# Kernel tuning notes

Hardware: AMD Instinct MI355X
Metric: run time of the kernel (lower is better)

The kernel has to match this reference:

```python
import jax, jax.numpy as jnp
import numpy as np

ACT_BITS = 8
W_BITS = 8
BN_EPS = 1e-5


def _round_ste(x):
    # straight-through round (HAWQ-style ste_round)
    return x + jax.lax.stop_gradient(jnp.round(x) - x)


def _quant_sym(x, bits):
    # symmetric per-tensor fake quantization; scale treated as constant (EMA min/max in original)
    n = float(2 ** (bits - 1) - 1)
    s = jax.lax.stop_gradient(jnp.maximum(jnp.max(jnp.abs(x)) / n, 1e-8))
    xq = jnp.clip(_round_ste(x / s), -n - 1.0, n) * s
    return xq, s


def _conv(x, w, stride, pad):
    return jax.lax.conv_general_dilated(
        x, w, (stride, stride), [(pad, pad), (pad, pad)],
        dimension_numbers=("NCHW", "OIHW", "NCHW"))


def _quant_bn(x, gamma, beta, mean, var):
    # fold BN into a per-channel scale+bias; quantize the folded scale like a weight
    ws = gamma * jax.lax.rsqrt(var + BN_EPS)          # [C]
    wq, ws_scale = _quant_sym(ws, W_BITS)
    b = beta - mean * wq                               # [C]
    return x * wq[None, :, None, None] + b[None, :, None, None], ws_scale


def setup_inputs() -> dict:
    key = jax.random.key(0)
    ks = jax.random.split(key, 16)
    d = {}
    d["x"] = jax.random.normal(ks[0], (32, 128, 56, 56), jnp.float32)
    d["w1"] = jax.random.normal(ks[1], (256, 128, 3, 3), jnp.float32) * 0.05
    d["w2"] = jax.random.normal(ks[2], (256, 256, 3, 3), jnp.float32) * 0.05
    d["w_id"] = jax.random.normal(ks[3], (256, 128, 1, 1), jnp.float32) * 0.05
    for i, pfx in enumerate(["bn1", "bn2", "id"]):
        k4 = jax.random.split(ks[4 + i], 4)
        d[pfx + "_gamma"] = jax.random.uniform(k4[0], (256,), jnp.float32) + 0.5
        d[pfx + "_beta"] = jax.random.normal(k4[1], (256,), jnp.float32) * 0.1
        d[pfx + "_mean"] = jax.random.normal(k4[2], (256,), jnp.float32) * 0.1
        d[pfx + "_var"] = jax.random.uniform(k4[3], (256,), jnp.float32) + 0.5
    return d


def reference(x, w1, w2, w_id,
              bn1_gamma, bn1_beta, bn1_mean, bn1_var,
              bn2_gamma, bn2_beta, bn2_mean, bn2_var,
              id_gamma, id_beta, id_mean, id_var):
    # quant_act on block input
    xq, act_s = _quant_sym(x, ACT_BITS)

    # identity branch: 1x1 stride-2 quantized conv -> quant_act -> folded quant bn
    w_id_q, _ = _quant_sym(w_id, W_BITS)
    identity = _conv(xq, w_id_q, 2, 0)
    identity, _ = _quant_sym(identity, ACT_BITS)
    identity, _ = _quant_bn(identity, id_gamma, id_beta, id_mean, id_var)

    # main branch conv1 (3x3 stride 2) -> act quant -> bn -> relu -> act quant
    w1_q, _ = _quant_sym(w1, W_BITS)
    h = _conv(xq, w1_q, 2, 1)
    h, _ = _quant_sym(h, ACT_BITS)
    h, _ = _quant_bn(h, bn1_gamma, bn1_beta, bn1_mean, bn1_var)
    h = jax.nn.relu(h)
    h, _ = _quant_sym(h, ACT_BITS)

    # conv2 (3x3 stride 1) -> act quant -> bn
    w2_q, _ = _quant_sym(w2, W_BITS)
    h = _conv(h, w2_q, 1, 1)
    h, _ = _quant_sym(h, ACT_BITS)
    h, _ = _quant_bn(h, bn2_gamma, bn2_beta, bn2_mean, bn2_var)

    # residual add -> int32 requant -> relu
    h = h + identity
    h, out_s = _quant_sym(h, ACT_BITS)
    h = jax.nn.relu(h)
    return h, out_s
```

## Files before the change

### kernel.cpp

```cpp
#include <hip/hip_runtime.h>
#include <limits.h>

#define THREADS 256

typedef int vi4 __attribute__((ext_vector_type(4)));

__device__ __forceinline__ float clamp8f(float q) { return fminf(fmaxf(q, -128.0f), 127.0f); }
__device__ __forceinline__ float sc_from_bits(unsigned b) {
  return fmaxf(__uint_as_float(b) / 127.0f, 1e-8f);
}
__device__ __forceinline__ signed char q8(float v, float s) {
  return (signed char)(int)clamp8f(rintf(v / s));
}


__device__ __forceinline__ void amax_body(const float4* __restrict__ p, int n4, int bid,
                                          int nblocks, int* __restrict__ slot) {
  const int tid = threadIdx.x;
  const int stride = nblocks * THREADS;
  float m = 0.0f;
  int i = bid * THREADS + tid;
  for (; i + 3 * stride < n4; i += 4 * stride) {
    float4 v0 = p[i];
    float4 v1 = p[i + stride];
    float4 v2 = p[i + 2 * stride];
    float4 v3 = p[i + 3 * stride];
    float m0 = fmaxf(fmaxf(fabsf(v0.x), fabsf(v0.y)), fmaxf(fabsf(v0.z), fabsf(v0.w)));
    float m1 = fmaxf(fmaxf(fabsf(v1.x), fabsf(v1.y)), fmaxf(fabsf(v1.z), fabsf(v1.w)));
    float m2 = fmaxf(fmaxf(fabsf(v2.x), fabsf(v2.y)), fmaxf(fabsf(v2.z), fabsf(v2.w)));
    float m3 = fmaxf(fmaxf(fabsf(v3.x), fabsf(v3.y)), fmaxf(fabsf(v3.z), fabsf(v3.w)));
    m = fmaxf(m, fmaxf(fmaxf(m0, m1), fmaxf(m2, m3)));
  }
  for (; i < n4; i += stride) {
    float4 v = p[i];
    m = fmaxf(m, fmaxf(fmaxf(fabsf(v.x), fabsf(v.y)), fmaxf(fabsf(v.z), fabsf(v.w))));
  }
#pragma unroll
  for (int k = 32; k >= 1; k >>= 1) m = fmaxf(m, __shfl_xor(m, k));
  __shared__ float wred[4];
  if ((tid & 63) == 0) wred[tid >> 6] = m;
  __syncthreads();
  if (tid == 0) {
    m = fmaxf(fmaxf(wred[0], wred[1]), fmaxf(wred[2], wred[3]));
    atomicMax(slot, __float_as_int(m));
  }
}

__global__ __launch_bounds__(THREADS) void k_pre(
    int* IS, const float* g1, const float* be1, const float* m1, const float* v1, float* wq1,
    float* b1, const float* g2, const float* be2, const float* m2, const float* v2, float* wq2,
    float* b2, const float* gi, const float* bei, const float* mi, const float* vvi, float* wqi,
    float* bi, const float4* w1, const float4* w2, const float4* wid, const float4* x) {
  int b = blockIdx.x;
  int c = threadIdx.x;
  if (b < 3) {
    const float *gamma, *beta, *mean, *var;
    float *wq, *bb;
    if (b == 0) { gamma = g1; beta = be1; mean = m1; var = v1; wq = wq1; bb = b1; }
    else if (b == 1) { gamma = g2; beta = be2; mean = m2; var = v2; wq = wq2; bb = b2; }
    else { gamma = gi; beta = bei; mean = mi; var = vvi; wq = wqi; bb = bi; }
    __shared__ float red[THREADS];
    float ws = gamma[c] * (1.0f / sqrtf(var[c] + 1e-5f));
    red[c] = fabsf(ws);
    __syncthreads();
    for (int s = THREADS / 2; s > 0; s >>= 1) {
      if (c < s) red[c] = fmaxf(red[c], red[c + s]);
      __syncthreads();
    }
    float sws = fmaxf(red[0] / 127.0f, 1e-8f);
    float q = clamp8f(rintf(ws / sws)) * sws;
    wq[c] = q;
    bb[c] = beta[c] - mean[c] * q;
    return;
  }
  b -= 3;
  if (b < 64) { amax_body(w1, 73728, b, 64, IS + 1); return; }
  b -= 64;
  if (b < 128) { amax_body(w2, 147456, b, 128, IS + 2); return; }
  b -= 128;
  if (b < 16) { amax_body(wid, 8192, b, 16, IS + 3); return; }
  b -= 16;
  amax_body(x, 3211264, b, 512, IS + 0);
}

__global__ __launch_bounds__(THREADS) void k_quant(const float* __restrict__ x,
                                                   int* __restrict__ X8,
                                                   const float* __restrict__ w1f,
                                                   vi4* __restrict__ W1m,
                                                   const float* __restrict__ w2f,
                                                   vi4* __restrict__ W2m,
                                                   const float* __restrict__ widf,
                                                   vi4* __restrict__ Widm,
                                                   const unsigned* __restrict__ ISu) {
  __shared__ signed char tile[56 * 132];
  int b = blockIdx.x;
  int t = threadIdx.x;
  if (b < 1792) {
    float s = sc_from_bits(ISu[0]);
    int h = b % 56, n = b / 56;
    const float* xp = x + ((n * 128) * 56 + h) * 56;
#pragma unroll
    for (int k = 0; k < 28; ++k) {
      int i = t + k * 256;
      int w = i % 56, c = i / 56;
      tile[w * 132 + c] = q8(xp[c * 3136 + w], s);
    }
    __syncthreads();
    int* op = X8 + (n * 56 + h) * 56 * 32;
#pragma unroll
    for (int k = 0; k < 7; ++k) {
      int i = t + k * 256;
      int w = i >> 5, c4 = (i & 31) * 4;
      const signed char* tp = tile + w * 132 + c4;
      op[i] = (int)(unsigned char)tp[0] | ((int)(unsigned char)tp[1] << 8) |
              ((int)(unsigned char)tp[2] << 16) | ((int)(unsigned char)tp[3] << 24);
    }
    return;
  }
  if (b < 1864) {
    int tt = (b - 1792) * THREADS + t;
    float s = sc_from_bits(ISu[1]);
    int lane = tt & 63;
    int cotile = (tt >> 6) & 15;
    int ks = tt >> 10;
    int tap = ks >> 1, kc = ks & 1;
    int kh = tap / 3, kw = tap % 3;
    int co = cotile * 16 + (lane & 15);
    int ci0 = kc * 64 + (lane >> 4) * 16;
    const float* src = w1f + (co * 128 + ci0) * 9 + kh * 3 + kw;
    int r[4];
#pragma unroll
    for (int q = 0; q < 4; ++q) {
      unsigned b0 = (unsigned char)q8(src[(q * 4 + 0) * 9], s);
      unsigned b1 = (unsigned char)q8(src[(q * 4 + 1) * 9], s);
      unsigned b2 = (unsigned char)q8(src[(q * 4 + 2) * 9], s);
      unsigned b3 = (unsigned char)q8(src[(q * 4 + 3) * 9], s);
      r[q] = (int)(b0 | (b1 << 8) | (b2 << 16) | (b3 << 24));
    }
    vi4 v = {r[0], r[1], r[2], r[3]};
    W1m[tt] = v;
    return;
  }
  if (b < 2008) {
    int tt = (b - 1864) * THREADS + t;
    float s = sc_from_bits(ISu[2]);
    int lane = tt & 63;
    int cotile = (tt >> 6) & 15;
    int ks = tt >> 10;
    int tap = ks >> 2, kc = ks & 3;
    int kh = tap / 3, kw = tap % 3;
    int co = cotile * 16 + (lane & 15);
    int ci0 = kc * 64 + (lane >> 4) * 16;
    const float* src = w2f + (co * 256 + ci0) * 9 + kh * 3 + kw;
    int r[4];
#pragma unroll
    for (int q = 0; q < 4; ++q) {
      unsigned b0 = (unsigned char)q8(src[(q * 4 + 0) * 9], s);
      unsigned b1 = (unsigned char)q8(src[(q * 4 + 1) * 9], s);
      unsigned b2 = (unsigned char)q8(src[(q * 4 + 2) * 9], s);
      unsigned b3 = (unsigned char)q8(src[(q * 4 + 3) * 9], s);
      r[q] = (int)(b0 | (b1 << 8) | (b2 << 16) | (b3 << 24));
    }
    vi4 v = {r[0], r[1], r[2], r[3]};
    W2m[tt] = v;
    return;
  }
  {
    int tt = (b - 2008) * THREADS + t;
    float s = sc_from_bits(ISu[3]);
    int lane = tt & 63;
    int cotile = (tt >> 6) & 15;
    int ks = tt >> 10;
    int co = cotile * 16 + (lane & 15);
    int ci0 = ks * 64 + (lane >> 4) * 16;
    const float* src = widf + co * 128 + ci0;
    int r[4];
#pragma unroll
    for (int q = 0; q < 4; ++q) {
      unsigned b0 = (unsigned char)q8(src[q * 4 + 0], s);
      unsigned b1 = (unsigned char)q8(src[q * 4 + 1], s);
      unsigned b2 = (unsigned char)q8(src[q * 4 + 2], s);
      unsigned b3 = (unsigned char)q8(src[q * 4 + 3], s);
      r[q] = (int)(b0 | (b1 << 8) | (b2 << 16) | (b3 << 24));
    }
    vi4 v = {r[0], r[1], r[2], r[3]};
    Widm[tt] = v;
  }
}

#define MFMA_I8(a, b, c) __builtin_amdgcn_mfma_i32_16x16x64_i8(a, b, c, 0, 0, 0)

__global__ __launch_bounds__(THREADS, 3) void k_conv1(const int* __restrict__ X8,
                                                      const vi4* __restrict__ W1m,
                                                      const vi4* __restrict__ Widm,
                                                      int* __restrict__ H1, int* __restrict__ IDI,
                                                      int* __restrict__ maxS,
                                                      int* __restrict__ minS,
                                                      int* __restrict__ maxabs_id) {
  __shared__ __align__(16) int lds[5 * 58 * 36];
  __shared__ int sMax[2][128], sMin[2][128], redA[4];
  const int tid = threadIdx.x;
  const int bx = blockIdx.x;
  const int n = bx / 28, rr = bx % 28;
  const int hp = rr >> 1, nh = rr & 1;
  const int ho0 = hp * 2;
  vi4 zero = {0, 0, 0, 0};

  for (int r = 0; r < 5; ++r) {
    int h = 2 * ho0 - 1 + r;
    int* dst = lds + r * 58 * 36;
    if (h >= 0 && h < 56) {
      const vi4* src = (const vi4*)(X8 + (n * 56 + h) * 56 * 32);
      for (int i4 = tid; i4 < 448; i4 += THREADS) {
        int col = i4 >> 3, c = (i4 & 7) * 4;
        *(vi4*)(dst + (col + 1) * 36 + c) = src[i4];
      }
      if (tid < 32) dst[tid] = 0;
      else if (tid >= 128 && tid < 160) dst[57 * 36 + (tid - 128)] = 0;
    } else {
      for (int i4 = tid; i4 < 522; i4 += THREADS) ((vi4*)dst)[i4] = zero;
    }
  }
  __syncthreads();

  const int lane = tid & 63, wv = tid >> 6;
  const int mw = wv & 1, nw = wv >> 1;
  const int lm = lane & 15, quad = lane >> 4;
  const int woc0 = lm, woc1 = (16 + lm) > 27 ? 27 : (16 + lm);
  const int choff = quad * 4;
  const int ho = ho0 + mw;
  const int obase = ((n * 28 + ho) * 28) * 256;
  const int ctbase = nh * 8 + nw * 4;

  vi4 acc[2][4];
  vi4 bA[4], bB[4];
  vi4 a0A, a1A, a0B, a1B;

#pragma unroll
  for (int mt = 0; mt < 2; ++mt)
#pragma unroll
    for (int ct = 0; ct < 4; ++ct) acc[mt][ct] = zero;
  const vi4* wibase = Widm + ctbase * 64 + lane;
  {
    const int ro = (2 * mw + 1) * 58;
#pragma unroll
    for (int kc = 0; kc < 2; ++kc) {
      vi4 a0 = *(const vi4*)(lds + (ro + 2 * woc0 + 1) * 36 + kc * 16 + choff);
      vi4 a1 = *(const vi4*)(lds + (ro + 2 * woc1 + 1) * 36 + kc * 16 + choff);
#pragma unroll
      for (int ct = 0; ct < 4; ++ct) {
        vi4 b = wibase[kc * 1024 + ct * 64];
        acc[0][ct] = MFMA_I8(a0, b, acc[0][ct]);
        acc[1][ct] = MFMA_I8(a1, b, acc[1][ct]);
      }
    }
  }
  int am = 0;
#pragma unroll
  for (int ct = 0; ct < 4; ++ct) {
    const int co = (ctbase + ct) * 16 + lm;
#pragma unroll
    for (int mt = 0; mt < 2; ++mt)
#pragma unroll
      for (int r = 0; r < 4; ++r) {
        int wo = mt * 16 + quad * 4 + r;
        if (wo < 28) {
          int v = acc[mt][ct][r];
          IDI[obase + wo * 256 + co] = v;
          am = max(am, v < 0 ? -v : v);
        }
      }
  }
#pragma unroll
  for (int k = 32; k >= 1; k >>= 1) am = max(am, __shfl_xor(am, k));
  if (lane == 0) redA[wv] = am;

#pragma unroll
  for (int mt = 0; mt < 2; ++mt)
#pragma unroll
    for (int ct = 0; ct < 4; ++ct) acc[mt][ct] = zero;
  const vi4* wbase = W1m + ctbase * 64 + lane;
#pragma unroll
  for (int ct = 0; ct < 4; ++ct) bA[ct] = wbase[ct * 64];
  {
    const int ro = (2 * mw) * 58;
    a0A = *(const vi4*)(lds + (ro + 2 * woc0) * 36 + choff);
    a1A = *(const vi4*)(lds + (ro + 2 * woc1) * 36 + choff);
  }
#pragma unroll 1
  for (int ks = 0; ks < 18; ks += 2) {
    {
      const int ksn = ks + 1;
      const int khn = (ksn >= 6) + (ksn >= 12);
      const int t2 = ksn - khn * 6;
      const int kwn = t2 >> 1, kcn = t2 & 1;
#pragma unroll
      for (int ct = 0; ct < 4; ++ct) bB[ct] = wbase[ksn * 1024 + ct * 64];
      const int ro = (2 * mw + khn) * 58;
      a0B = *(const vi4*)(lds + (ro + 2 * woc0 + kwn) * 36 + kcn * 16 + choff);
      a1B = *(const vi4*)(lds + (ro + 2 * woc1 + kwn) * 36 + kcn * 16 + choff);
    }
#pragma unroll
    for (int ct = 0; ct < 4; ++ct) {
      acc[0][ct] = MFMA_I8(a0A, bA[ct], acc[0][ct]);
      acc[1][ct] = MFMA_I8(a1A, bA[ct], acc[1][ct]);
    }
    if (ks + 2 < 18) {
      const int ksn = ks + 2;
      const int khn = (ksn >= 6) + (ksn >= 12);
      const int t2 = ksn - khn * 6;
      const int kwn = t2 >> 1, kcn = t2 & 1;
#pragma unroll
      for (int ct = 0; ct < 4; ++ct) bA[ct] = wbase[ksn * 1024 + ct * 64];
      const int ro = (2 * mw + khn) * 58;
      a0A = *(const vi4*)(lds + (ro + 2 * woc0 + kwn) * 36 + kcn * 16 + choff);
      a1A = *(const vi4*)(lds + (ro + 2 * woc1 + kwn) * 36 + kcn * 16 + choff);
    }
#pragma unroll
    for (int ct = 0; ct < 4; ++ct) {
      acc[0][ct] = MFMA_I8(a0B, bB[ct], acc[0][ct]);
      acc[1][ct] = MFMA_I8(a1B, bB[ct], acc[1][ct]);
    }
  }

#pragma unroll
  for (int ct = 0; ct < 4; ++ct) {
    const int co = (ctbase + ct) * 16 + lm;
    int vmax = INT_MIN, vmin = INT_MAX;
#pragma unroll
    for (int mt = 0; mt < 2; ++mt)
#pragma unroll
      for (int r = 0; r < 4; ++r) {
        int wo = mt * 16 + quad * 4 + r;
        if (wo < 28) {
          int v = acc[mt][ct][r];
          H1[obase + wo * 256 + co] = v;
          vmax = max(vmax, v);
          vmin = min(vmin, v);
        }
      }
    vmax = max(vmax, __shfl_xor(vmax, 16));
    vmax = max(vmax, __shfl_xor(vmax, 32));
    vmin = min(vmin, __shfl_xor(vmin, 16));
    vmin = min(vmin, __shfl_xor(vmin, 32));
    if (lane < 16) {
      sMax[mw][nw * 64 + ct * 16 + lane] = vmax;
      sMin[mw][nw * 64 + ct * 16 + lane] = vmin;
    }
  }
  __syncthreads();
  if (tid < 128) {
    int row = n * 14 + hp;
    maxS[row * 256 + nh * 128 + tid] = max(sMax[0][tid], sMax[1][tid]);
    minS[row * 256 + nh * 128 + tid] = min(sMin[0][tid], sMin[1][tid]);
  }
  if (tid == 0) {
    int a = max(max(redA[0], redA[1]), max(redA[2], redA[3]));
    atomicMax(maxabs_id, a);
  }
}

__global__ __launch_bounds__(1024) void k_rs1(int* __restrict__ IS, float* __restrict__ SC,
                                              const int* __restrict__ maxS,
                                              const int* __restrict__ minS,
                                              const float* __restrict__ wq1,
                                              const float* __restrict__ b1) {
  __shared__ int pMax[4][256], pMin[4][256];
  __shared__ int ri[256];
  __shared__ float rf[256];
  int t = threadIdx.x;
  int c = t & 255, part = t >> 8;
  int vmax = INT_MIN, vmin = INT_MAX;
#pragma unroll 4
  for (int r = part; r < 448; r += 4) {
    vmax = max(vmax, maxS[r * 256 + c]);
    vmin = min(vmin, minS[r * 256 + c]);
  }
  pMax[part][c] = vmax;
  pMin[part][c] = vmin;
  __syncthreads();
  if (t < 256) {
    vmax = max(max(pMax[0][c], pMax[1][c]), max(pMax[2][c], pMax[3][c]));
    vmin = min(min(pMin[0][c], pMin[1][c]), min(pMin[2][c], pMin[3][c]));
    int a1 = vmax < 0 ? -vmax : vmax;
    int a0 = vmin < 0 ? -vmin : vmin;
    ri[c] = max(a1, a0);
  }
  __syncthreads();
  for (int s = 128; s > 0; s >>= 1) {
    if (t < s) ri[t] = max(ri[t], ri[t + s]);
    __syncthreads();
  }
  int mh1 = ri[0];
  const unsigned* ISu = (const unsigned*)IS;
  float sx = sc_from_bits(ISu[0]);
  float sw1 = sc_from_bits(ISu[1]);
  float sxw = sx * sw1;
  float s_h1 = fmaxf(sxw * (float)mh1 / 127.0f, 1e-8f);
  if (t < 256) {
    float wq = wq1[c], bbc = b1[c];
    float q1 = clamp8f(rintf((float)vmax * sxw / s_h1));
    float q0 = clamp8f(rintf((float)vmin * sxw / s_h1));
    float hv1 = q1 * s_h1, hv0 = q0 * s_h1;
    float y1 = fmaxf(hv1 * wq + bbc, 0.0f);
    float y0 = fmaxf(hv0 * wq + bbc, 0.0f);
    rf[c] = fmaxf(y1, y0);
  }
  __syncthreads();
  for (int s = 128; s > 0; s >>= 1) {
    if (t < s) rf[t] = fmaxf(rf[t], rf[t + s]);
    __syncthreads();
  }
  if (t == 0) {
    IS[4] = mh1;
    SC[7] = rf[0];
    SC[8] = s_h1;
    SC[9] = fmaxf(rf[0] / 127.0f, 1e-8f);
    float swid = sc_from_bits(ISu[3]);
    SC[10] = fmaxf(sx * swid * (float)IS[5] / 127.0f, 1e-8f);
  }
}

__device__ __forceinline__ signed char qact(int v, float sxw, float s_h1, float s_y2, float wq,
                                            float bb) {
  float hf = (float)v * sxw;
  float q = clamp8f(rintf(hf / s_h1));
  float hv = q * s_h1;
  float y = fmaxf(hv * wq + bb, 0.0f);
  float a = fminf(fmaxf(rintf(y / s_y2), -128.0f), 127.0f);
  return (signed char)(int)a;
}

__global__ __launch_bounds__(THREADS) void k_qh1(const int4* __restrict__ H1,
                                                 char4* __restrict__ A2,
                                                 const float* __restrict__ SC,
                                                 const float* __restrict__ wq1,
                                                 const float* __restrict__ b1) {
  int t = blockIdx.x * THREADS + threadIdx.x;
  const unsigned* ISu = (const unsigned*)SC;
  float sx = sc_from_bits(ISu[0]);
  float sw1 = sc_from_bits(ISu[1]);
  float sxw = sx * sw1;
  float s_h1 = SC[8];
  float s_y2 = SC[9];
  int4 v = H1[t];
  int c0 = (t * 4) & 255;
  char4 r;
  r.x = qact(v.x, sxw, s_h1, s_y2, wq1[c0], b1[c0]);
  r.y = qact(v.y, sxw, s_h1, s_y2, wq1[c0 + 1], b1[c0 + 1]);
  r.z = qact(v.z, sxw, s_h1, s_y2, wq1[c0 + 2], b1[c0 + 2]);
  r.w = qact(v.w, sxw, s_h1, s_y2, wq1[c0 + 3], b1[c0 + 3]);
  A2[t] = r;
}

__global__ __launch_bounds__(THREADS, 4) void k_conv2(const int* __restrict__ A2,
                                                      const vi4* __restrict__ W2m,
                                                      int* __restrict__ H2,
                                                      int* __restrict__ maxabs_h2) {
  __shared__ __align__(16) int lds[4 * 30 * 68];
  __shared__ int redA[4];
  const int tid = threadIdx.x;
  const int bx = blockIdx.x;
  const int n = bx / 28, rr = bx % 28;
  const int hp = rr >> 1, nh = rr & 1;
  const int ho0 = hp * 2;
  vi4 zero = {0, 0, 0, 0};

  for (int r = 0; r < 4; ++r) {
    int h = ho0 - 1 + r;
    int* dst = lds + r * 30 * 68;
    if (h >= 0 && h < 28) {
      const vi4* src = (const vi4*)(A2 + (n * 28 + h) * 28 * 64);
      for (int i4 = tid; i4 < 448; i4 += THREADS) {
        int col = i4 >> 4, c = (i4 & 15) * 4;
        *(vi4*)(dst + (col + 1) * 68 + c) = src[i4];
      }
      if (tid < 64) dst[tid] = 0;
      else if (tid >= 128 && tid < 192) dst[29 * 68 + (tid - 128)] = 0;
    } else {
      for (int i4 = tid; i4 < 510; i4 += THREADS) ((vi4*)dst)[i4] = zero;
    }
  }
  __syncthreads();

  const int lane = tid & 63, wv = tid >> 6;
  const int mw = wv & 1, nw = wv >> 1;
  const int lm = lane & 15, quad = lane >> 4;
  const int woc0 = lm, woc1 = (16 + lm) > 27 ? 27 : (16 + lm);
  const int choff = quad * 4;
  const int ho = ho0 + mw;
  const int ctbase = nh * 8 + nw * 4;

  vi4 acc[2][4];
  vi4 bA[4], bB[4];
  vi4 a0A, a1A, a0B, a1B;
#pragma unroll
  for (int mt = 0; mt < 2; ++mt)
#pragma unroll
    for (int ct = 0; ct < 4; ++ct) acc[mt][ct] = zero;

  const vi4* wbase = W2m + ctbase * 64 + lane;
#pragma unroll
  for (int ct = 0; ct < 4; ++ct) bA[ct] = wbase[ct * 64];
  {
    const int ro = mw * 30;
    a0A = *(const vi4*)(lds + (ro + woc0) * 68 + choff);
    a1A = *(const vi4*)(lds + (ro + woc1) * 68 + choff);
  }
#pragma unroll 1
  for (int ks = 0; ks < 36; ks += 2) {
    {
      const int ksn = ks + 1;
      const int khn = (ksn >= 12) + (ksn >= 24);
      const int t2 = ksn - khn * 12;
      const int kwn = t2 >> 2, kcn = t2 & 3;
#pragma unroll
      for (int ct = 0; ct < 4; ++ct) bB[ct] = wbase[ksn * 1024 + ct * 64];
      const int ro = (mw + khn) * 30;
      a0B = *(const vi4*)(lds + (ro + woc0 + kwn) * 68 + kcn * 16 + choff);
      a1B = *(const vi4*)(lds + (ro + woc1 + kwn) * 68 + kcn * 16 + choff);
    }
#pragma unroll
    for (int ct = 0; ct < 4; ++ct) {
      acc[0][ct] = MFMA_I8(a0A, bA[ct], acc[0][ct]);
      acc[1][ct] = MFMA_I8(a1A, bA[ct], acc[1][ct]);
    }
    if (ks + 2 < 36) {
      const int ksn = ks + 2;
      const int khn = (ksn >= 12) + (ksn >= 24);
      const int t2 = ksn - khn * 12;
      const int kwn = t2 >> 2, kcn = t2 & 3;
#pragma unroll
      for (int ct = 0; ct < 4; ++ct) bA[ct] = wbase[ksn * 1024 + ct * 64];
      const int ro = (mw + khn) * 30;
      a0A = *(const vi4*)(lds + (ro + woc0 + kwn) * 68 + kcn * 16 + choff);
      a1A = *(const vi4*)(lds + (ro + woc1 + kwn) * 68 + kcn * 16 + choff);
    }
#pragma unroll
    for (int ct = 0; ct < 4; ++ct) {
      acc[0][ct] = MFMA_I8(a0B, bB[ct], acc[0][ct]);
      acc[1][ct] = MFMA_I8(a1B, bB[ct], acc[1][ct]);
    }
  }

  const int obase = ((n * 28 + ho) * 28) * 256;
  int am = 0;
#pragma unroll
  for (int ct = 0; ct < 4; ++ct) {
    const int co = (ctbase + ct) * 16 + lm;
#pragma unroll
    for (int mt = 0; mt < 2; ++mt)
#pragma unroll
      for (int r = 0; r < 4; ++r) {
        int wo = mt * 16 + quad * 4 + r;
        if (wo < 28) {
          int v = acc[mt][ct][r];
          H2[obase + wo * 256 + co] = v;
          am = max(am, v < 0 ? -v : v);
        }
      }
  }
#pragma unroll
  for (int k = 32; k >= 1; k >>= 1) am = max(am, __shfl_xor(am, k));
  if (lane == 0) redA[wv] = am;
  __syncthreads();
  if (tid == 0) {
    int a = max(max(redA[0], redA[1]), max(redA[2], redA[3]));
    atomicMax(maxabs_h2, a);
  }
}

struct SumParams {
  float sxw2, s_h2, sxwid, s_idq;
};
__device__ __forceinline__ float sum_val(int v2, int vi, const SumParams& P, float wq2c, float b2c,
                                         float wqidc, float bidc) {
  float q2 = clamp8f(rintf((float)v2 * P.sxw2 / P.s_h2));
  float z = (q2 * P.s_h2) * wq2c + b2c;
  float qi = clamp8f(rintf((float)vi * P.sxwid / P.s_idq));
  float zi = (qi * P.s_idq) * wqidc + bidc;
  return z + zi;
}
__device__ __forceinline__ SumParams make_params(const float* SC, const int* IS) {
  const unsigned* ISu = (const unsigned*)IS;
  SumParams P;
  float sx = sc_from_bits(ISu[0]);
  float sw2 = sc_from_bits(ISu[2]);
  float swid = sc_from_bits(ISu[3]);
  float s_y2 = SC[9];
  P.s_idq = SC[10];
  P.sxw2 = s_y2 * sw2;
  P.s_h2 = fmaxf(P.sxw2 * (float)IS[6] / 127.0f, 1e-8f);
  P.sxwid = sx * swid;
  return P;
}

__global__ __launch_bounds__(THREADS) void k_absmax2(const int4* __restrict__ H2,
                                                     const int4* __restrict__ IDI,
                                                     const float* __restrict__ SC,
                                                     const int* __restrict__ IS,
                                                     const float* __restrict__ wq2,
                                                     const float* __restrict__ b2,
                                                     const float* __restrict__ wqid,
                                                     const float* __restrict__ bidp,
                                                     int* __restrict__ slot) {
  __shared__ float pw2[256], pb2[256], pwi[256], pbi[256];
  int tid = threadIdx.x;
  pw2[tid] = wq2[tid];
  pb2[tid] = b2[tid];
  pwi[tid] = wqid[tid];
  pbi[tid] = bidp[tid];
  __syncthreads();
  SumParams P = make_params(SC, IS);
  const int n4 = 1605632;
  const int stride = gridDim.x * THREADS;
  float m = 0.0f;
  for (int i = blockIdx.x * THREADS + tid; i < n4; i += stride) {
    int4 v2 = H2[i];
    int4 vi = IDI[i];
    int c0 = (i * 4) & 255;
    m = fmaxf(m, fabsf(sum_val(v2.x, vi.x, P, pw2[c0], pb2[c0], pwi[c0], pbi[c0])));
    m = fmaxf(m, fabsf(sum_val(v2.y, vi.y, P, pw2[c0 + 1], pb2[c0 + 1], pwi[c0 + 1], pbi[c0 + 1])));
    m = fmaxf(m, fabsf(sum_val(v2.z, vi.z, P, pw2[c0 + 2], pb2[c0 + 2], pwi[c0 + 2], pbi[c0 + 2])));
    m = fmaxf(m, fabsf(sum_val(v2.w, vi.w, P, pw2[c0 + 3], pb2[c0 + 3], pwi[c0 + 3], pbi[c0 + 3])));
  }
#pragma unroll
  for (int k = 32; k >= 1; k >>= 1) m = fmaxf(m, __shfl_xor(m, k));
  __shared__ float wred[4];
  if ((tid & 63) == 0) wred[tid >> 6] = m;
  __syncthreads();
  if (tid == 0) {
    m = fmaxf(fmaxf(wred[0], wred[1]), fmaxf(wred[2], wred[3]));
    atomicMax(slot, __float_as_int(m));
  }
}

__global__ __launch_bounds__(THREADS) void k_out(const int* __restrict__ H2,
                                                 const int* __restrict__ IDI,
                                                 const float* __restrict__ SC,
                                                 const int* __restrict__ IS,
                                                 const float* __restrict__ wq2,
                                                 const float* __restrict__ b2,
                                                 const float* __restrict__ wqid,
                                                 const float* __restrict__ bidp,
                                                 float* __restrict__ out) {
  __shared__ float tile[64 * 57];
  __shared__ float pw2[64], pb2[64], pwi[64], pbi[64];
  int tid = threadIdx.x;
  int b = blockIdx.x;
  int ct = b & 3;
  int rt = (b >> 2) % 14;
  int n = b / 56;
  int c0 = ct * 64;
  int r0 = rt * 56;
  if (tid < 64) {
    pw2[tid] = wq2[c0 + tid];
    pb2[tid] = b2[c0 + tid];
    pwi[tid] = wqid[c0 + tid];
    pbi[tid] = bidp[c0 + tid];
  }
  __syncthreads();
  SumParams P = make_params(SC, IS);
  float out_s = fmaxf(__uint_as_float(((const unsigned*)IS)[11]) / 127.0f, 1e-8f);

  const int base = (n * 784 + r0) * 256 + c0;
#pragma unroll
  for (int k = 0; k < 14; ++k) {
    int idx = tid + k * 256;
    int rl = idx >> 6;
    int cl = idx & 63;
    int e = base + rl * 256 + cl;
    float sv = sum_val(H2[e], IDI[e], P, pw2[cl], pb2[cl], pwi[cl], pbi[cl]);
    float q = clamp8f(rintf(sv / out_s));
    tile[cl * 57 + rl] = q > 0.0f ? q * out_s : 0.0f;
  }
  __syncthreads();
  float* ob = out + n * 200704 + c0 * 784 + r0;
#pragma unroll
  for (int k = 0; k < 14; ++k) {
    int idx = tid + k * 256;
    int cl = idx / 56;
    int rl = idx % 56;
    ob[cl * 784 + rl] = tile[cl * 57 + rl];
  }
  if (b == 0 && tid == 0) out[6422528] = out_s;
}

extern "C" void kernel_launch(void* const* d_in, const int* in_sizes, int n_in, void* d_out,
                              int out_size, void* d_ws, size_t ws_size, hipStream_t stream) {
  (void)in_sizes; (void)n_in; (void)out_size; (void)ws_size;
  const float* x = (const float*)d_in[0];
  const float* w1 = (const float*)d_in[1];
  const float* w2 = (const float*)d_in[2];
  const float* wid = (const float*)d_in[3];
  const float* bn1g = (const float*)d_in[4];
  const float* bn1b = (const float*)d_in[5];
  const float* bn1m = (const float*)d_in[6];
  const float* bn1v = (const float*)d_in[7];
  const float* bn2g = (const float*)d_in[8];
  const float* bn2b = (const float*)d_in[9];
  const float* bn2m = (const float*)d_in[10];
  const float* bn2v = (const float*)d_in[11];
  const float* idg = (const float*)d_in[12];
  const float* idb = (const float*)d_in[13];
  const float* idm = (const float*)d_in[14];
  const float* idv = (const float*)d_in[15];

  char* ws = (char*)d_ws;
  float* SC = (float*)ws;
  int* IS = (int*)ws;
  unsigned* ISu = (unsigned*)ws;
  float* wq1 = (float*)(ws + 3072);
  float* b1 = (float*)(ws + 4096);
  float* wq2 = (float*)(ws + 5120);
  float* b2 = (float*)(ws + 6144);
  float* wqid = (float*)(ws + 7168);
  float* bid = (float*)(ws + 8192);
  char* X8 = ws + 16384;
  char* A2 = X8;
  char* W1m = X8 + 12845056;
  char* W2m = W1m + 294912;
  char* Widm = W2m + 589824;
  int* H1 = (int*)(Widm + 32768);
  int* H2 = H1;
  int* IDI = (int*)((char*)H1 + 25690112);
  float* out = (float*)d_out;
  int* maxS = (int*)d_out;
  int* minS = maxS + 448 * 256;

  k_pre<<<723, THREADS, 0, stream>>>(IS, bn1g, bn1b, bn1m, bn1v, wq1, b1, bn2g, bn2b, bn2m, bn2v,
                                     wq2, b2, idg, idb, idm, idv, wqid, bid, (const float4*)w1,
                                     (const float4*)w2, (const float4*)wid, (const float4*)x);
  k_quant<<<2016, THREADS, 0, stream>>>(x, (int*)X8, w1, (vi4*)W1m, w2, (vi4*)W2m, wid,
                                        (vi4*)Widm, ISu);
  k_conv1<<<896, THREADS, 0, stream>>>((const int*)X8, (const vi4*)W1m, (const vi4*)Widm, H1, IDI,
                                       maxS, minS, IS + 5);
  k_rs1<<<1, 1024, 0, stream>>>(IS, SC, maxS, minS, wq1, b1);
  k_qh1<<<6272, THREADS, 0, stream>>>((const int4*)H1, (char4*)A2, SC, wq1, b1);
  k_conv2<<<896, THREADS, 0, stream>>>((const int*)A2, (const vi4*)W2m, H2, IS + 6);
  k_absmax2<<<1024, THREADS, 0, stream>>>((const int4*)H2, (const int4*)IDI, SC, IS, wq2, b2, wqid,
                                          bid, IS + 11);
  k_out<<<1792, THREADS, 0, stream>>>(H2, IDI, SC, IS, wq2, b2, wqid, bid, out);
}
```

Baseline: 253.3 us.

## Fuse conv2, residual absmax and output into one grid-synced persistent kernel

Merges conv2, the residual-sum absmax pass and the output quantization kernel into a single kernel. Accumulators stay in registers across two software grid barriers built from atomic counters with spin-waits, so the int32 H2 tensor is never written to or re-read from global memory. This relies on all 896 blocks being co-resident on the GPU, otherwise it deadlocks. The counters are reset inside k_rs1.

```diff
diff --git a/kernel.cpp b/kernel.cpp
--- a/kernel.cpp
+++ b/kernel.cpp
@@ -2,6 +2,7 @@
 #include <limits.h>
 
 #define THREADS 256
+#define TAIL_BLOCKS 896
 
 typedef int vi4 __attribute__((ext_vector_type(4)));
 
@@ -418,6 +419,8 @@
     SC[9] = fmaxf(rf[0] / 127.0f, 1e-8f);
     float swid = sc_from_bits(ISu[3]);
     SC[10] = fmaxf(sx * swid * (float)IS[5] / 127.0f, 1e-8f);
+    IS[64] = 0;
+    IS[65] = 0;
   }
 }
 
@@ -453,12 +456,44 @@
   A2[t] = r;
 }
 
-__global__ __launch_bounds__(THREADS, 4) void k_conv2(const int* __restrict__ A2,
-                                                      const vi4* __restrict__ W2m,
-                                                      int* __restrict__ H2,
-                                                      int* __restrict__ maxabs_h2) {
+struct SumParams {
+  float sxw2, s_h2, sxwid, s_idq;
+};
+__device__ __forceinline__ float sum_val(int v2, int vi, const SumParams& P, float wq2c, float b2c,
+                                         float wqidc, float bidc) {
+  float q2 = clamp8f(rintf((float)v2 * P.sxw2 / P.s_h2));
+  float z = (q2 * P.s_h2) * wq2c + b2c;
+  float qi = clamp8f(rintf((float)vi * P.sxwid / P.s_idq));
+  float zi = (qi * P.s_idq) * wqidc + bidc;
+  return z + zi;
+}
+__device__ __forceinline__ SumParams make_params2(const float* SC, const unsigned* ISu, int mh2) {
+  SumParams P;
+  float sx = sc_from_bits(ISu[0]);
+  float sw2 = sc_from_bits(ISu[2]);
+  float swid = sc_from_bits(ISu[3]);
+  float s_y2 = SC[9];
+  P.s_idq = SC[10];
+  P.sxw2 = s_y2 * sw2;
+  P.s_h2 = fmaxf(P.sxw2 * (float)mh2 / 127.0f, 1e-8f);
+  P.sxwid = sx * swid;
+  return P;
+}
+
+__global__ __launch_bounds__(THREADS, 4) void k_tail(const int* __restrict__ A2,
+                                                     const vi4* __restrict__ W2m,
+                                                     const int* __restrict__ IDI,
+                                                     const float* SC, int* IS,
+                                                     const float* __restrict__ wq2,
+                                                     const float* __restrict__ b2,
+                                                     const float* __restrict__ wqid,
+                                                     const float* __restrict__ bidp,
+                                                     float* __restrict__ out) {
   __shared__ __align__(16) int lds[4 * 30 * 68];
   __shared__ int redA[4];
+  __shared__ float redF[4];
+  __shared__ int sMh2;
+  __shared__ float sOutS;
   const int tid = threadIdx.x;
   const int bx = blockIdx.x;
   const int n = bx / 28, rr = bx % 28;
@@ -488,7 +523,6 @@
   const int lm = lane & 15, quad = lane >> 4;
   const int woc0 = lm, woc1 = (16 + lm) > 27 ? 27 : (16 + lm);
   const int choff = quad * 4;
-  const int ho = ho0 + mw;
   const int ctbase = nh * 8 + nw * 4;
 
   vi4 acc[2][4];
@@ -543,11 +577,9 @@
     }
   }
 
-  const int obase = ((n * 28 + ho) * 28) * 256;
   int am = 0;
 #pragma unroll
-  for (int ct = 0; ct < 4; ++ct) {
-    const int co = (ctbase + ct) * 16 + lm;
+  for (int ct = 0; ct < 4; ++ct)
 #pragma unroll
     for (int mt = 0; mt < 2; ++mt)
 #pragma unroll
@@ -555,135 +587,83 @@
         int wo = mt * 16 + quad * 4 + r;
         if (wo < 28) {
           int v = acc[mt][ct][r];
-          H2[obase + wo * 256 + co] = v;
           am = max(am, v < 0 ? -v : v);
         }
       }
-  }
 #pragma unroll
   for (int k = 32; k >= 1; k >>= 1) am = max(am, __shfl_xor(am, k));
   if (lane == 0) redA[wv] = am;
   __syncthreads();
   if (tid == 0) {
     int a = max(max(redA[0], redA[1]), max(redA[2], redA[3]));
-    atomicMax(maxabs_h2, a);
-  }
-}
-
-struct SumParams {
-  float sxw2, s_h2, sxwid, s_idq;
-};
-__device__ __forceinline__ float sum_val(int v2, int vi, const SumParams& P, float wq2c, float b2c,
-                                         float wqidc, float bidc) {
-  float q2 = clamp8f(rintf((float)v2 * P.sxw2 / P.s_h2));
-  float z = (q2 * P.s_h2) * wq2c + b2c;
-  float qi = clamp8f(rintf((float)vi * P.sxwid / P.s_idq));
-  float zi = (qi * P.s_idq) * wqidc + bidc;
-  return z + zi;
-}
-__device__ __forceinline__ SumParams make_params(const float* SC, const int* IS) {
-  const unsigned* ISu = (const unsigned*)IS;
-  SumParams P;
-  float sx = sc_from_bits(ISu[0]);
-  float sw2 = sc_from_bits(ISu[2]);
-  float swid = sc_from_bits(ISu[3]);
-  float s_y2 = SC[9];
-  P.s_idq = SC[10];
-  P.sxw2 = s_y2 * sw2;
-  P.s_h2 = fmaxf(P.sxw2 * (float)IS[6] / 127.0f, 1e-8f);
-  P.sxwid = sx * swid;
-  return P;
-}
-
-__global__ __launch_bounds__(THREADS) void k_absmax2(const int4* __restrict__ H2,
-                                                     const int4* __restrict__ IDI,
-                                                     const float* __restrict__ SC,
-                                                     const int* __restrict__ IS,
-                                                     const float* __restrict__ wq2,
-                                                     const float* __restrict__ b2,
-                                                     const float* __restrict__ wqid,
-                                                     const float* __restrict__ bidp,
-                                                     int* __restrict__ slot) {
-  __shared__ float pw2[256], pb2[256], pwi[256], pbi[256];
-  int tid = threadIdx.x;
-  pw2[tid] = wq2[tid];
-  pb2[tid] = b2[tid];
-  pwi[tid] = wqid[tid];
-  pbi[tid] = bidp[tid];
-  __syncthreads();
-  SumParams P = make_params(SC, IS);
-  const int n4 = 1605632;
-  const int stride = gridDim.x * THREADS;
-  float m = 0.0f;
-  for (int i = blockIdx.x * THREADS + tid; i < n4; i += stride) {
-    int4 v2 = H2[i];
-    int4 vi = IDI[i];
-    int c0 = (i * 4) & 255;
-    m = fmaxf(m, fabsf(sum_val(v2.x, vi.x, P, pw2[c0], pb2[c0], pwi[c0], pbi[c0])));
-    m = fmaxf(m, fabsf(sum_val(v2.y, vi.y, P, pw2[c0 + 1], pb2[c0 + 1], pwi[c0 + 1], pbi[c0 + 1])));
-    m = fmaxf(m, fabsf(sum_val(v2.z, vi.z, P, pw2[c0 + 2], pb2[c0 + 2], pwi[c0 + 2], pbi[c0 + 2])));
-    m = fmaxf(m, fabsf(sum_val(v2.w, vi.w, P, pw2[c0 + 3], pb2[c0 + 3], pwi[c0 + 3], pbi[c0 + 3])));
-  }
-#pragma unroll
-  for (int k = 32; k >= 1; k >>= 1) m = fmaxf(m, __shfl_xor(m, k));
-  __shared__ float wred[4];
-  if ((tid & 63) == 0) wred[tid >> 6] = m;
+    atomicMax(IS + 6, a);
+  }
+
+  int* sumsi = lds;
+  float* sums = (float*)lds;
+  const int ib = ((n * 28 + ho0) * 28) * 256 + nh * 128;
+#pragma unroll
+  for (int k = 0; k < 28; ++k) {
+    int idx = tid + k * 256;
+    int cl = idx & 127, sp = idx >> 7;
+    sumsi[cl * 57 + sp] = IDI[ib + sp * 256 + cl];
+  }
+
   __syncthreads();
   if (tid == 0) {
-    m = fmaxf(fmaxf(wred[0], wred[1]), fmaxf(wred[2], wred[3]));
-    atomicMax(slot, __float_as_int(m));
-  }
-}
-
-__global__ __launch_bounds__(THREADS) void k_out(const int* __restrict__ H2,
-                                                 const int* __restrict__ IDI,
-                                                 const float* __restrict__ SC,
-                                                 const int* __restrict__ IS,
-                                                 const float* __restrict__ wq2,
-                                                 const float* __restrict__ b2,
-                                                 const float* __restrict__ wqid,
-                                                 const float* __restrict__ bidp,
-                                                 float* __restrict__ out) {
-  __shared__ float tile[64 * 57];
-  __shared__ float pw2[64], pb2[64], pwi[64], pbi[64];
-  int tid = threadIdx.x;
-  int b = blockIdx.x;
-  int ct = b & 3;
-  int rt = (b >> 2) % 14;
-  int n = b / 56;
-  int c0 = ct * 64;
-  int r0 = rt * 56;
-  if (tid < 64) {
-    pw2[tid] = wq2[c0 + tid];
-    pb2[tid] = b2[c0 + tid];
-    pwi[tid] = wqid[c0 + tid];
-    pbi[tid] = bidp[c0 + tid];
-  }
-  __syncthreads();
-  SumParams P = make_params(SC, IS);
-  float out_s = fmaxf(__uint_as_float(((const unsigned*)IS)[11]) / 127.0f, 1e-8f);
-
-  const int base = (n * 784 + r0) * 256 + c0;
-#pragma unroll
-  for (int k = 0; k < 14; ++k) {
+    __hip_atomic_fetch_add(IS + 64, 1, __ATOMIC_RELEASE, __HIP_MEMORY_SCOPE_AGENT);
+    while (__hip_atomic_load(IS + 64, __ATOMIC_ACQUIRE, __HIP_MEMORY_SCOPE_AGENT) < TAIL_BLOCKS)
+      __builtin_amdgcn_s_sleep(8);
+    sMh2 = atomicMax(IS + 6, INT_MIN);
+  }
+  __syncthreads();
+  const SumParams P = make_params2(SC, (const unsigned*)IS, sMh2);
+
+  float fm = 0.0f;
+#pragma unroll
+  for (int ct = 0; ct < 4; ++ct) {
+    const int co = (ctbase + ct) * 16 + lm;
+    const int cl = co - nh * 128;
+    float w2c = wq2[co], b2c = b2[co], wic = wqid[co], bic = bidp[co];
+#pragma unroll
+    for (int mt = 0; mt < 2; ++mt)
+#pragma unroll
+      for (int r = 0; r < 4; ++r) {
+        int wo = mt * 16 + quad * 4 + r;
+        if (wo < 28) {
+          int slot = cl * 57 + mw * 28 + wo;
+          float sv = sum_val(acc[mt][ct][r], sumsi[slot], P, w2c, b2c, wic, bic);
+          sums[slot] = sv;
+          fm = fmaxf(fm, fabsf(sv));
+        }
+      }
+  }
+#pragma unroll
+  for (int k = 32; k >= 1; k >>= 1) fm = fmaxf(fm, __shfl_xor(fm, k));
+  if (lane == 0) redF[wv] = fm;
+  __syncthreads();
+
+  if (tid == 0) {
+    float a = fmaxf(fmaxf(redF[0], redF[1]), fmaxf(redF[2], redF[3]));
+    atomicMax(IS + 11, __float_as_int(a));
+    __hip_atomic_fetch_add(IS + 65, 1, __ATOMIC_RELEASE, __HIP_MEMORY_SCOPE_AGENT);
+    while (__hip_atomic_load(IS + 65, __ATOMIC_ACQUIRE, __HIP_MEMORY_SCOPE_AGENT) < TAIL_BLOCKS)
+      __builtin_amdgcn_s_sleep(8);
+    sOutS = fmaxf(__int_as_float(atomicMax(IS + 11, INT_MIN)) / 127.0f, 1e-8f);
+  }
+  __syncthreads();
+  const float out_s = sOutS;
+
+  float* ob = out + n * 200704 + (nh * 128) * 784 + ho0 * 28;
+#pragma unroll
+  for (int k = 0; k < 28; ++k) {
     int idx = tid + k * 256;
-    int rl = idx >> 6;
-    int cl = idx & 63;
-    int e = base + rl * 256 + cl;
-    float sv = sum_val(H2[e], IDI[e], P, pw2[cl], pb2[cl], pwi[cl], pbi[cl]);
+    int cl = idx / 56, rem = idx % 56;
+    float sv = sums[cl * 57 + rem];
     float q = clamp8f(rintf(sv / out_s));
-    tile[cl * 57 + rl] = q > 0.0f ? q * out_s : 0.0f;
-  }
-  __syncthreads();
-  float* ob = out + n * 200704 + c0 * 784 + r0;
-#pragma unroll
-  for (int k = 0; k < 14; ++k) {
-    int idx = tid + k * 256;
-    int cl = idx / 56;
-    int rl = idx % 56;
-    ob[cl * 784 + rl] = tile[cl * 57 + rl];
-  }
-  if (b == 0 && tid == 0) out[6422528] = out_s;
+    ob[cl * 784 + rem] = q > 0.0f ? q * out_s : 0.0f;
+  }
+  if (bx == 0 && tid == 0) out[6422528] = out_s;
 }
 
 extern "C" void kernel_launch(void* const* d_in, const int* in_sizes, int n_in, void* d_out,
@@ -722,7 +702,6 @@
   char* W2m = W1m + 294912;
   char* Widm = W2m + 589824;
   int* H1 = (int*)(Widm + 32768);
-  int* H2 = H1;
   int* IDI = (int*)((char*)H1 + 25690112);
   float* out = (float*)d_out;
   int* maxS = (int*)d_out;
@@ -737,8 +716,6 @@
                                        maxS, minS, IS + 5);
   k_rs1<<<1, 1024, 0, stream>>>(IS, SC, maxS, minS, wq1, b1);
   k_qh1<<<6272, THREADS, 0, stream>>>((const int4*)H1, (char4*)A2, SC, wq1, b1);
-  k_conv2<<<896, THREADS, 0, stream>>>((const int*)A2, (const vi4*)W2m, H2, IS + 6);
-  k_absmax2<<<1024, THREADS, 0, stream>>>((const int4*)H2, (const int4*)IDI, SC, IS, wq2, b2, wqid,
-                                          bid, IS + 11);
-  k_out<<<1792, THREADS, 0, stream>>>(H2, IDI, SC, IS, wq2, b2, wqid, bid, out);
-}
+  k_tail<<<TAIL_BLOCKS, THREADS, 0, stream>>>((const int*)A2, (const vi4*)W2m, (const int*)IDI, SC,
+                                              IS, wq2, b2, wqid, bid, out);
+}
```

Result: slower. 475.7 us (+87.8%).
